# Performance work log

Hardware: AMD Instinct MI355X
Metric: run time of the kernel (lower is better)

The kernel has to match this reference:

```python
import jax, jax.numpy as jnp
import numpy as np

N_NODES = 50000
N_EDGES = 800000
N_GRAPHS = 256
D_IN = 128
D_HID = 128


def setup_inputs() -> dict:
    key = jax.random.key(0)
    ks = jax.random.split(key, 10)
    x = jax.random.normal(ks[0], (N_NODES, D_IN), dtype=jnp.float32)
    edge_index = jax.random.randint(ks[1], (2, N_EDGES), 0, N_NODES, dtype=jnp.int64)
    batch = jnp.sort(jax.random.randint(ks[2], (N_NODES,), 0, N_GRAPHS, dtype=jnp.int64))
    def lin(k, din, dout):
        s = 1.0 / np.sqrt(din)
        return jax.random.uniform(k, (din, dout), jnp.float32, -s, s)
    W1 = lin(ks[3], D_IN, D_HID); b1 = jnp.zeros((D_HID,), jnp.float32)
    W2 = lin(ks[4], D_HID, D_HID); b2 = jnp.zeros((D_HID,), jnp.float32)
    W3 = lin(ks[5], D_HID, D_HID); b3 = jnp.zeros((D_HID,), jnp.float32)
    return {"x": x, "edge_index": edge_index, "batch": batch,
            "W1": W1, "b1": b1, "W2": W2, "b2": b2, "W3": W3, "b3": b3}


def _gcn_norm(edge_index, num_nodes):
    # PyG gcn_norm with add_self_loops=True, edge_weight=1
    loops = jnp.arange(num_nodes, dtype=edge_index.dtype)
    src = jnp.concatenate([edge_index[0], loops])
    dst = jnp.concatenate([edge_index[1], loops])
    ones = jnp.ones(src.shape[0], jnp.float32)
    deg = jax.ops.segment_sum(ones, dst, num_segments=num_nodes)
    dinv = jnp.where(deg > 0, jax.lax.rsqrt(deg), 0.0)
    norm = dinv[src] * dinv[dst]
    return src, dst, norm


def _gcn_conv(x, src, dst, norm, W, b, num_nodes):
    h = x @ W                              # [N, dout] transform first
    msg = h[src] * norm[:, None]           # gather + scale  [E+N, dout]
    agg = jax.ops.segment_sum(msg, dst, num_segments=num_nodes)
    return agg + b


def reference(x, edge_index, batch, W1, b1, W2, b2, W3, b3):
    n = x.shape[0]
    src, dst, norm = _gcn_norm(edge_index, n)
    h = jax.nn.relu(_gcn_conv(x, src, dst, norm, W1, b1, n))
    h = jax.nn.relu(_gcn_conv(h, src, dst, norm, W2, b2, n))
    h = _gcn_conv(h, src, dst, norm, W3, b3, n)
    # global_mean_pool over batch ids
    sums = jax.ops.segment_sum(h, batch, num_segments=N_GRAPHS)
    cnts = jax.ops.segment_sum(jnp.ones((n,), jnp.float32), batch, num_segments=N_GRAPHS)
    return sums / jnp.maximum(cnts, 1.0)[:, None]
```

## Files before the change

kernel.cpp:

```cpp
#include <hip/hip_runtime.h>

#define N_NODES 50000
#define N_PAD   50048
#define N_EDGES 800000
#define N_GRAPHS 256
#define D 128
#define CAP 64
#define MFMA_GRID (N_PAD / 128)

#define NBUCK 196
#define BCAP  4608
#define EPB_I4 512
#define NBLK_A ((N_EDGES / 4 + EPB_I4 - 1) / EPB_I4)

typedef short bf16x8 __attribute__((ext_vector_type(8)));
typedef float f32x4  __attribute__((ext_vector_type(4)));

__device__ inline unsigned short f2bf(float f) {
    unsigned u = __float_as_uint(f);
    u += 0x7FFF + ((u >> 16) & 1);
    return (unsigned short)(u >> 16);
}
__device__ inline float bf2f(unsigned short b) { return __uint_as_float((unsigned)b << 16); }

__global__ __launch_bounds__(256) void k_pack(const float* __restrict__ W1, const float* __restrict__ W2,
                                              const float* __restrict__ W3, unsigned short* __restrict__ Wp) {
    int idx = blockIdx.x * 256 + threadIdx.x;
    if (idx >= 3 * D * D) return;
    int L = idx >> 14, rem = idx & 16383;
    int k = rem >> 7, n = rem & 127;
    const float* W = (L == 0) ? W1 : (L == 1) ? W2 : W3;
    float w = W[k * D + n];
    int kt = k >> 5, kg = (k >> 3) & 3, i = k & 7;
    int nt = n >> 4, ln = kg * 16 + (n & 15);
    size_t dst = (size_t)L * 32768 + ((size_t)(kt * 8 + nt) * 64 + ln) * 8 + i;
    unsigned short hi = f2bf(w);
    Wp[dst]         = hi;
    Wp[dst + 16384] = f2bf(w - bf2f(hi));
}


__global__ __launch_bounds__(256) void k_part(const int* __restrict__ ei, int* __restrict__ cursor,
                                              unsigned* __restrict__ buck) {
    __shared__ int hist[NBUCK];
    __shared__ int lbase[NBUCK];
    for (int i = threadIdx.x; i < NBUCK; i += 256) hist[i] = 0;
    __syncthreads();

    const int4* s4 = reinterpret_cast<const int4*>(ei);
    const int4* d4 = reinterpret_cast<const int4*>(ei + N_EDGES);
    int idx0 = blockIdx.x * EPB_I4 + threadIdx.x;
    int idx1 = idx0 + 256;
    bool v0 = idx0 < N_EDGES / 4, v1 = idx1 < N_EDGES / 4;
    int4 d0 = {}, d1 = {}, s0 = {}, s1 = {};
    if (v0) {
        d0 = d4[idx0]; s0 = s4[idx0];
        atomicAdd(&hist[d0.x >> 8], 1); atomicAdd(&hist[d0.y >> 8], 1);
        atomicAdd(&hist[d0.z >> 8], 1); atomicAdd(&hist[d0.w >> 8], 1);
    }
    if (v1) {
        d1 = d4[idx1]; s1 = s4[idx1];
        atomicAdd(&hist[d1.x >> 8], 1); atomicAdd(&hist[d1.y >> 8], 1);
        atomicAdd(&hist[d1.z >> 8], 1); atomicAdd(&hist[d1.w >> 8], 1);
    }
    __syncthreads();

    for (int i = threadIdx.x; i < NBUCK; i += 256)
        lbase[i] = atomicAdd(&cursor[i], hist[i]);
    __syncthreads();

    auto put = [&](int d, int s) {
        int b = d >> 8;
        int p = atomicAdd(&lbase[b], 1);
        if (p < BCAP) buck[(size_t)b * BCAP + p] = ((unsigned)(d & 255) << 16) | (unsigned)s;
    };
    if (v0) { put(d0.x, s0.x); put(d0.y, s0.y); put(d0.z, s0.z); put(d0.w, s0.w); }
    if (v1) { put(d1.x, s1.x); put(d1.y, s1.y); put(d1.z, s1.z); put(d1.w, s1.w); }
}


__global__ __launch_bounds__(256) void k_build(const unsigned* __restrict__ buck,
                                               const int* __restrict__ cursor,
                                               int* __restrict__ cnt, unsigned short* __restrict__ colu) {
    __shared__ int lcnt[256];
    int b = blockIdx.x;
    lcnt[threadIdx.x] = 0;
    __syncthreads();
    int nE = min(cursor[b], BCAP);
    const unsigned* bb = buck + (size_t)b * BCAP;
    for (int i = threadIdx.x; i < nE; i += 256) {
        unsigned v = bb[i];
        int dl = v >> 16, s = v & 0xFFFF;
        int p = atomicAdd(&lcnt[dl], 1);
        if (p < CAP) colu[(size_t)(b * 256 + dl) * CAP + p] = (unsigned short)s;
    }
    __syncthreads();
    int node = b * 256 + threadIdx.x;
    if (node < N_NODES) cnt[node] = lcnt[threadIdx.x];
}


template<bool F32IN>
__global__ __launch_bounds__(512) void k_mfma(const void* __restrict__ Ain,
                                              const unsigned short* __restrict__ Wp,
                                              const int* __restrict__ cnt,
                                              unsigned short* __restrict__ T) {
    __shared__ uint4 Wl[4096];
    const uint4* wp4 = reinterpret_cast<const uint4*>(Wp);
    for (int i = threadIdx.x; i < 4096; i += 512) Wl[i] = wp4[i];
    __syncthreads();

    int l  = threadIdx.x & 63;
    int wv = threadIdx.x >> 6;
    int row0 = blockIdx.x * 128 + wv * 16;
    int arow = row0 + (l & 15);
    int kchunk = l >> 4;

    f32x4 acc[8] = {};
    #pragma unroll
    for (int s = 0; s < 4; ++s) {
        bf16x8 af;
        if (F32IN) {
            float4 a0 = {}, a1 = {};
            if (arow < N_NODES) {
                const float* xr = (const float*)Ain + (size_t)arow * D + s * 32 + kchunk * 8;
                a0 = reinterpret_cast<const float4*>(xr)[0];
                a1 = reinterpret_cast<const float4*>(xr)[1];
            }
            unsigned short h[8] = { f2bf(a0.x), f2bf(a0.y), f2bf(a0.z), f2bf(a0.w),
                                    f2bf(a1.x), f2bf(a1.y), f2bf(a1.z), f2bf(a1.w) };
            __builtin_memcpy(&af, h, 16);
        } else {
            const unsigned short* ar = (const unsigned short*)Ain + (size_t)arow * D;
            uint4 av = reinterpret_cast<const uint4*>(ar)[s * 4 + kchunk];
            __builtin_memcpy(&af, &av, 16);
        }
        #pragma unroll
        for (int nt = 0; nt < 8; ++nt) {
            int f = s * 8 + nt;
            uint4 bh = Wl[f * 64 + l];
            uint4 bl = Wl[f * 64 + l + 2048];
            bf16x8 bhf, blf;
            __builtin_memcpy(&bhf, &bh, 16);
            __builtin_memcpy(&blf, &bl, 16);
            acc[nt] = __builtin_amdgcn_mfma_f32_16x16x32_bf16(af, bhf, acc[nt], 0, 0, 0);
            acc[nt] = __builtin_amdgcn_mfma_f32_16x16x32_bf16(af, blf, acc[nt], 0, 0, 0);
        }
    }

    int rbase = row0 + (l >> 4) * 4;
    int cr = l & 15;
    float sc[4];
    #pragma unroll
    for (int j = 0; j < 4; ++j) {
        int rr = rbase + j;
        sc[j] = (rr < N_NODES) ? rsqrtf((float)cnt[rr] + 1.f) : 0.f;
    }
    #pragma unroll
    for (int nt = 0; nt < 8; ++nt)
        #pragma unroll
        for (int j = 0; j < 4; ++j) {
            int rr = rbase + j;
            if (rr < N_NODES) T[(size_t)rr * D + nt * 16 + cr] = f2bf(acc[nt][j] * sc[j]);
        }
}


template<bool LAST>
__global__ __launch_bounds__(256) void k_agg(const unsigned* __restrict__ Tu,
                                             unsigned* __restrict__ Anext, const float* __restrict__ bias,
                                             const int* __restrict__ cnt, const unsigned short* __restrict__ colu) {
    int node = blockIdx.x * 4 + (threadIdx.x >> 6);
    int lane = threadIdx.x & 63;
    if (node >= N_NODES) return;

    int len = cnt[node];
    float dd = rsqrtf((float)len + 1.f);
    unsigned ts = Tu[(size_t)node * 64 + lane];
    float2 acc;
    acc.x = __uint_as_float(ts << 16);
    acc.y = __uint_as_float(ts & 0xFFFF0000u);

    const unsigned short* crow = colu + (size_t)node * CAP;
    int j = 0;
    for (; j + 8 <= len; j += 8) {
        uint4 c = *reinterpret_cast<const uint4*>(crow + j);
        int s0 = c.x & 0xFFFF, s1 = c.x >> 16;
        int s2 = c.y & 0xFFFF, s3 = c.y >> 16;
        int s4 = c.z & 0xFFFF, s5 = c.z >> 16;
        int s6 = c.w & 0xFFFF, s7 = c.w >> 16;
        unsigned t0 = Tu[(size_t)s0 * 64 + lane];
        unsigned t1 = Tu[(size_t)s1 * 64 + lane];
        unsigned t2 = Tu[(size_t)s2 * 64 + lane];
        unsigned t3 = Tu[(size_t)s3 * 64 + lane];
        unsigned t4 = Tu[(size_t)s4 * 64 + lane];
        unsigned t5 = Tu[(size_t)s5 * 64 + lane];
        unsigned t6 = Tu[(size_t)s6 * 64 + lane];
        unsigned t7 = Tu[(size_t)s7 * 64 + lane];
        acc.x += __uint_as_float(t0 << 16); acc.y += __uint_as_float(t0 & 0xFFFF0000u);
        acc.x += __uint_as_float(t1 << 16); acc.y += __uint_as_float(t1 & 0xFFFF0000u);
        acc.x += __uint_as_float(t2 << 16); acc.y += __uint_as_float(t2 & 0xFFFF0000u);
        acc.x += __uint_as_float(t3 << 16); acc.y += __uint_as_float(t3 & 0xFFFF0000u);
        acc.x += __uint_as_float(t4 << 16); acc.y += __uint_as_float(t4 & 0xFFFF0000u);
        acc.x += __uint_as_float(t5 << 16); acc.y += __uint_as_float(t5 & 0xFFFF0000u);
        acc.x += __uint_as_float(t6 << 16); acc.y += __uint_as_float(t6 & 0xFFFF0000u);
        acc.x += __uint_as_float(t7 << 16); acc.y += __uint_as_float(t7 & 0xFFFF0000u);
    }
    for (; j < len; ++j) {
        int s = crow[j];
        unsigned t0 = Tu[(size_t)s * 64 + lane];
        acc.x += __uint_as_float(t0 << 16); acc.y += __uint_as_float(t0 & 0xFFFF0000u);
    }

    acc.x *= dd; acc.y *= dd;
    if (!LAST) {
        acc.x = fmaxf(acc.x + bias[2 * lane], 0.f);
        acc.y = fmaxf(acc.y + bias[2 * lane + 1], 0.f);
    }
    Anext[(size_t)node * 64 + lane] = (unsigned)f2bf(acc.x) | ((unsigned)f2bf(acc.y) << 16);
}


__global__ __launch_bounds__(128) void k_pool(const unsigned short* __restrict__ AGGb,
                                              const float* __restrict__ b3,
                                              const int* __restrict__ batch, float* __restrict__ out) {
    int g = blockIdx.x;
    int c = threadIdx.x;
    int beg, end;
    { int lo = 0, hi = N_NODES; while (lo < hi) { int m = (lo + hi) >> 1; if (batch[m] < g) lo = m + 1; else hi = m; } beg = lo; }
    { int lo = beg, hi = N_NODES; while (lo < hi) { int m = (lo + hi) >> 1; if (batch[m] < g + 1) lo = m + 1; else hi = m; } end = lo; }
    float acc = 0.f;
    #pragma unroll 4
    for (int i = beg; i < end; ++i) acc += bf2f(AGGb[(size_t)i * D + c]);
    int n = end - beg;
    out[g * D + c] = (acc + (float)n * b3[c]) / (float)(n > 0 ? n : 1);
}


static inline size_t align256(size_t x) { return (x + 255) & ~(size_t)255; }

extern "C" void kernel_launch(void* const* d_in, const int* in_sizes, int n_in,
                              void* d_out, int out_size, void* d_ws, size_t ws_size,
                              hipStream_t stream) {
    const float* x    = (const float*)d_in[0];
    const int*  ei    = (const int*)d_in[1];
    const int*  batch = (const int*)d_in[2];
    const float* W1 = (const float*)d_in[3];
    const float* b1 = (const float*)d_in[4];
    const float* W2 = (const float*)d_in[5];
    const float* b2 = (const float*)d_in[6];
    const float* W3 = (const float*)d_in[7];
    const float* b3 = (const float*)d_in[8];
    float* out = (float*)d_out;

    char* ws = (char*)d_ws;
    size_t off = 0;
    auto alloc = [&](size_t bytes) { void* p = ws + off; off = align256(off + bytes); return p; };
    int*      cursor = (int*)     alloc((size_t)NBUCK * 4);
    unsigned* buck   = (unsigned*)alloc((size_t)NBUCK * BCAP * 4);
    int*      cnt    = (int*)     alloc((size_t)N_NODES * 4);
    unsigned short* colu = (unsigned short*)alloc((size_t)NBUCK * 256 * CAP * 2);
    unsigned short* Wp = (unsigned short*)alloc((size_t)3 * 32768 * 2);
    unsigned short* Ab = (unsigned short*)alloc((size_t)N_PAD * D * 2);
    unsigned short* T  = (unsigned short*)alloc((size_t)N_PAD * D * 2);
    (void)ws_size; (void)in_sizes; (void)n_in; (void)out_size;

    hipMemsetAsync(cursor, 0, (size_t)NBUCK * 4, stream);

    k_pack <<<(3 * D * D + 255) / 256, 256, 0, stream>>>(W1, W2, W3, Wp);
    k_part <<<NBLK_A, 256, 0, stream>>>(ei, cursor, buck);
    k_build<<<NBUCK, 256, 0, stream>>>(buck, cursor, cnt, colu);

    const int agg_grid = (N_NODES + 3) / 4;

    k_mfma<true ><<<MFMA_GRID, 512, 0, stream>>>(x,  Wp,         cnt, T);
    k_agg<false><<<agg_grid, 256, 0, stream>>>((const unsigned*)T, (unsigned*)Ab, b1, cnt, colu);
    k_mfma<false><<<MFMA_GRID, 512, 0, stream>>>(Ab, Wp + 32768, cnt, T);
    k_agg<false><<<agg_grid, 256, 0, stream>>>((const unsigned*)T, (unsigned*)Ab, b2, cnt, colu);
    k_mfma<false><<<MFMA_GRID, 512, 0, stream>>>(Ab, Wp + 65536, cnt, T);
    k_agg<true ><<<agg_grid, 256, 0, stream>>>((const unsigned*)T, (unsigned*)Ab, nullptr, cnt, colu);
    k_pool <<<N_GRAPHS, 128, 0, stream>>>(Ab, b3, batch, out);
}
```

Before: 276.3 us.

## Fuse last aggregation with mean pool, merge pack/partition, two nodes per wave

Merges the weight-pack and edge-partition kernels into one launch by splitting the block range. The aggregation kernel now handles two nodes per wavefront, interleaving their gathers so more loads are in flight. The final aggregation is fused into the pooling kernel: each graph block aggregates its own nodes and reduces directly, so the third layer's output is never written and reread. The cost is that the fused pool kernel runs only 256 blocks, one per graph, which may underuse the GPU for the last gather.

```diff
diff --git a/kernel.cpp b/kernel.cpp
--- a/kernel.cpp
+++ b/kernel.cpp
@@ -12,6 +12,7 @@
 #define BCAP  4608
 #define EPB_I4 512
 #define NBLK_A ((N_EDGES / 4 + EPB_I4 - 1) / EPB_I4)
+#define PACK_BLKS 192
 
 typedef short bf16x8 __attribute__((ext_vector_type(8)));
 typedef float f32x4  __attribute__((ext_vector_type(4)));
@@ -22,34 +23,59 @@
     return (unsigned short)(u >> 16);
 }
 __device__ inline float bf2f(unsigned short b) { return __uint_as_float((unsigned)b << 16); }
-
-__global__ __launch_bounds__(256) void k_pack(const float* __restrict__ W1, const float* __restrict__ W2,
-                                              const float* __restrict__ W3, unsigned short* __restrict__ Wp) {
-    int idx = blockIdx.x * 256 + threadIdx.x;
-    if (idx >= 3 * D * D) return;
-    int L = idx >> 14, rem = idx & 16383;
-    int k = rem >> 7, n = rem & 127;
-    const float* W = (L == 0) ? W1 : (L == 1) ? W2 : W3;
-    float w = W[k * D + n];
-    int kt = k >> 5, kg = (k >> 3) & 3, i = k & 7;
-    int nt = n >> 4, ln = kg * 16 + (n & 15);
-    size_t dst = (size_t)L * 32768 + ((size_t)(kt * 8 + nt) * 64 + ln) * 8 + i;
-    unsigned short hi = f2bf(w);
-    Wp[dst]         = hi;
-    Wp[dst + 16384] = f2bf(w - bf2f(hi));
-}
-
-
-__global__ __launch_bounds__(256) void k_part(const int* __restrict__ ei, int* __restrict__ cursor,
-                                              unsigned* __restrict__ buck) {
+__device__ inline float bflo(unsigned t) { return __uint_as_float(t << 16); }
+__device__ inline float bfhi(unsigned t) { return __uint_as_float(t & 0xFFFF0000u); }
+
+__device__ inline void gather8(const unsigned* __restrict__ Tu, const unsigned short* __restrict__ crow,
+                               int j, int lane, float2& acc) {
+    uint4 c = *reinterpret_cast<const uint4*>(crow + j);
+    unsigned t0 = Tu[(size_t)(c.x & 0xFFFF) * 64 + lane];
+    unsigned t1 = Tu[(size_t)(c.x >> 16)    * 64 + lane];
+    unsigned t2 = Tu[(size_t)(c.y & 0xFFFF) * 64 + lane];
+    unsigned t3 = Tu[(size_t)(c.y >> 16)    * 64 + lane];
+    unsigned t4 = Tu[(size_t)(c.z & 0xFFFF) * 64 + lane];
+    unsigned t5 = Tu[(size_t)(c.z >> 16)    * 64 + lane];
+    unsigned t6 = Tu[(size_t)(c.w & 0xFFFF) * 64 + lane];
+    unsigned t7 = Tu[(size_t)(c.w >> 16)    * 64 + lane];
+    acc.x += bflo(t0); acc.y += bfhi(t0);
+    acc.x += bflo(t1); acc.y += bfhi(t1);
+    acc.x += bflo(t2); acc.y += bfhi(t2);
+    acc.x += bflo(t3); acc.y += bfhi(t3);
+    acc.x += bflo(t4); acc.y += bfhi(t4);
+    acc.x += bflo(t5); acc.y += bfhi(t5);
+    acc.x += bflo(t6); acc.y += bfhi(t6);
+    acc.x += bflo(t7); acc.y += bfhi(t7);
+}
+
+
+__global__ __launch_bounds__(256) void k_packpart(const float* __restrict__ W1, const float* __restrict__ W2,
+                                                  const float* __restrict__ W3, unsigned short* __restrict__ Wp,
+                                                  const int* __restrict__ ei, int* __restrict__ cursor,
+                                                  unsigned* __restrict__ buck) {
+    if (blockIdx.x < PACK_BLKS) {
+        int idx = blockIdx.x * 256 + threadIdx.x;
+        int L = idx >> 14, rem = idx & 16383;
+        int k = rem >> 7, n = rem & 127;
+        const float* W = (L == 0) ? W1 : (L == 1) ? W2 : W3;
+        float w = W[k * D + n];
+        int kt = k >> 5, kg = (k >> 3) & 3, i = k & 7;
+        int nt = n >> 4, ln = kg * 16 + (n & 15);
+        size_t dst = (size_t)L * 32768 + ((size_t)(kt * 8 + nt) * 64 + ln) * 8 + i;
+        unsigned short hi = f2bf(w);
+        Wp[dst]         = hi;
+        Wp[dst + 16384] = f2bf(w - bf2f(hi));
+        return;
+    }
+
     __shared__ int hist[NBUCK];
     __shared__ int lbase[NBUCK];
     for (int i = threadIdx.x; i < NBUCK; i += 256) hist[i] = 0;
     __syncthreads();
 
+    int pb = blockIdx.x - PACK_BLKS;
     const int4* s4 = reinterpret_cast<const int4*>(ei);
     const int4* d4 = reinterpret_cast<const int4*>(ei + N_EDGES);
-    int idx0 = blockIdx.x * EPB_I4 + threadIdx.x;
+    int idx0 = pb * EPB_I4 + threadIdx.x;
     int idx1 = idx0 + 256;
     bool v0 = idx0 < N_EDGES / 4, v1 = idx1 < N_EDGES / 4;
     int4 d0 = {}, d1 = {}, s0 = {}, s1 = {};
@@ -166,74 +192,88 @@
 }
 
 
-template<bool LAST>
 __global__ __launch_bounds__(256) void k_agg(const unsigned* __restrict__ Tu,
                                              unsigned* __restrict__ Anext, const float* __restrict__ bias,
                                              const int* __restrict__ cnt, const unsigned short* __restrict__ colu) {
-    int node = blockIdx.x * 4 + (threadIdx.x >> 6);
+    int wid  = (blockIdx.x * 256 + threadIdx.x) >> 6;
     int lane = threadIdx.x & 63;
-    if (node >= N_NODES) return;
-
-    int len = cnt[node];
-    float dd = rsqrtf((float)len + 1.f);
-    unsigned ts = Tu[(size_t)node * 64 + lane];
-    float2 acc;
-    acc.x = __uint_as_float(ts << 16);
-    acc.y = __uint_as_float(ts & 0xFFFF0000u);
-
-    const unsigned short* crow = colu + (size_t)node * CAP;
+    int n0 = wid * 2;
+    if (n0 >= N_NODES) return;
+    int n1 = n0 + 1;
+
+    int len0 = cnt[n0], len1 = cnt[n1];
+    int lim0 = min(len0, CAP), lim1 = min(len1, CAP);
+    unsigned ts0 = Tu[(size_t)n0 * 64 + lane];
+    unsigned ts1 = Tu[(size_t)n1 * 64 + lane];
+    float2 A0, A1;
+    A0.x = bflo(ts0); A0.y = bfhi(ts0);
+    A1.x = bflo(ts1); A1.y = bfhi(ts1);
+
+    const unsigned short* r0 = colu + (size_t)n0 * CAP;
+    const unsigned short* r1 = colu + (size_t)n1 * CAP;
+    int m = min(lim0, lim1);
     int j = 0;
-    for (; j + 8 <= len; j += 8) {
-        uint4 c = *reinterpret_cast<const uint4*>(crow + j);
-        int s0 = c.x & 0xFFFF, s1 = c.x >> 16;
-        int s2 = c.y & 0xFFFF, s3 = c.y >> 16;
-        int s4 = c.z & 0xFFFF, s5 = c.z >> 16;
-        int s6 = c.w & 0xFFFF, s7 = c.w >> 16;
-        unsigned t0 = Tu[(size_t)s0 * 64 + lane];
-        unsigned t1 = Tu[(size_t)s1 * 64 + lane];
-        unsigned t2 = Tu[(size_t)s2 * 64 + lane];
-        unsigned t3 = Tu[(size_t)s3 * 64 + lane];
-        unsigned t4 = Tu[(size_t)s4 * 64 + lane];
-        unsigned t5 = Tu[(size_t)s5 * 64 + lane];
-        unsigned t6 = Tu[(size_t)s6 * 64 + lane];
-        unsigned t7 = Tu[(size_t)s7 * 64 + lane];
-        acc.x += __uint_as_float(t0 << 16); acc.y += __uint_as_float(t0 & 0xFFFF0000u);
-        acc.x += __uint_as_float(t1 << 16); acc.y += __uint_as_float(t1 & 0xFFFF0000u);
-        acc.x += __uint_as_float(t2 << 16); acc.y += __uint_as_float(t2 & 0xFFFF0000u);
-        acc.x += __uint_as_float(t3 << 16); acc.y += __uint_as_float(t3 & 0xFFFF0000u);
-        acc.x += __uint_as_float(t4 << 16); acc.y += __uint_as_float(t4 & 0xFFFF0000u);
-        acc.x += __uint_as_float(t5 << 16); acc.y += __uint_as_float(t5 & 0xFFFF0000u);
-        acc.x += __uint_as_float(t6 << 16); acc.y += __uint_as_float(t6 & 0xFFFF0000u);
-        acc.x += __uint_as_float(t7 << 16); acc.y += __uint_as_float(t7 & 0xFFFF0000u);
-    }
-    for (; j < len; ++j) {
-        int s = crow[j];
-        unsigned t0 = Tu[(size_t)s * 64 + lane];
-        acc.x += __uint_as_float(t0 << 16); acc.y += __uint_as_float(t0 & 0xFFFF0000u);
-    }
-
-    acc.x *= dd; acc.y *= dd;
-    if (!LAST) {
-        acc.x = fmaxf(acc.x + bias[2 * lane], 0.f);
-        acc.y = fmaxf(acc.y + bias[2 * lane + 1], 0.f);
-    }
-    Anext[(size_t)node * 64 + lane] = (unsigned)f2bf(acc.x) | ((unsigned)f2bf(acc.y) << 16);
-}
-
-
-__global__ __launch_bounds__(128) void k_pool(const unsigned short* __restrict__ AGGb,
-                                              const float* __restrict__ b3,
-                                              const int* __restrict__ batch, float* __restrict__ out) {
+    for (; j + 8 <= m; j += 8) {
+        gather8(Tu, r0, j, lane, A0);
+        gather8(Tu, r1, j, lane, A1);
+    }
+    int ja = j;
+    for (; ja + 8 <= lim0; ja += 8) gather8(Tu, r0, ja, lane, A0);
+    for (; ja < lim0; ++ja) { unsigned t = Tu[(size_t)r0[ja] * 64 + lane]; A0.x += bflo(t); A0.y += bfhi(t); }
+    int jb = j;
+    for (; jb + 8 <= lim1; jb += 8) gather8(Tu, r1, jb, lane, A1);
+    for (; jb < lim1; ++jb) { unsigned t = Tu[(size_t)r1[jb] * 64 + lane]; A1.x += bflo(t); A1.y += bfhi(t); }
+
+    float dd0 = rsqrtf((float)len0 + 1.f);
+    float dd1 = rsqrtf((float)len1 + 1.f);
+    float bx = bias[2 * lane], by = bias[2 * lane + 1];
+    float r0x = fmaxf(A0.x * dd0 + bx, 0.f), r0y = fmaxf(A0.y * dd0 + by, 0.f);
+    float r1x = fmaxf(A1.x * dd1 + bx, 0.f), r1y = fmaxf(A1.y * dd1 + by, 0.f);
+    Anext[(size_t)n0 * 64 + lane] = (unsigned)f2bf(r0x) | ((unsigned)f2bf(r0y) << 16);
+    Anext[(size_t)n1 * 64 + lane] = (unsigned)f2bf(r1x) | ((unsigned)f2bf(r1y) << 16);
+}
+
+
+__global__ __launch_bounds__(1024) void k_aggpool(const unsigned* __restrict__ Tu,
+                                                  const int* __restrict__ cnt,
+                                                  const unsigned short* __restrict__ colu,
+                                                  const int* __restrict__ batch,
+                                                  const float* __restrict__ b3,
+                                                  float* __restrict__ out) {
     int g = blockIdx.x;
-    int c = threadIdx.x;
     int beg, end;
     { int lo = 0, hi = N_NODES; while (lo < hi) { int m = (lo + hi) >> 1; if (batch[m] < g) lo = m + 1; else hi = m; } beg = lo; }
     { int lo = beg, hi = N_NODES; while (lo < hi) { int m = (lo + hi) >> 1; if (batch[m] < g + 1) lo = m + 1; else hi = m; } end = lo; }
-    float acc = 0.f;
-    #pragma unroll 4
-    for (int i = beg; i < end; ++i) acc += bf2f(AGGb[(size_t)i * D + c]);
-    int n = end - beg;
-    out[g * D + c] = (acc + (float)n * b3[c]) / (float)(n > 0 ? n : 1);
+    int lane = threadIdx.x & 63, wv = threadIdx.x >> 6;
+
+    float2 psum = make_float2(0.f, 0.f);
+    for (int node = beg + wv; node < end; node += 16) {
+        int len = cnt[node];
+        int lim = min(len, CAP);
+        unsigned ts = Tu[(size_t)node * 64 + lane];
+        float2 acc;
+        acc.x = bflo(ts); acc.y = bfhi(ts);
+        const unsigned short* crow = colu + (size_t)node * CAP;
+        int j = 0;
+        for (; j + 8 <= lim; j += 8) gather8(Tu, crow, j, lane, acc);
+        for (; j < lim; ++j) { unsigned t = Tu[(size_t)crow[j] * 64 + lane]; acc.x += bflo(t); acc.y += bfhi(t); }
+        float dd = rsqrtf((float)len + 1.f);
+        psum.x += acc.x * dd;
+        psum.y += acc.y * dd;
+    }
+
+    __shared__ float2 red[16][64];
+    red[wv][lane] = psum;
+    __syncthreads();
+    if (wv == 0) {
+        float2 s = red[0][lane];
+        #pragma unroll
+        for (int w = 1; w < 16; ++w) { s.x += red[w][lane].x; s.y += red[w][lane].y; }
+        int n = end - beg;
+        float inv = 1.f / (float)(n > 0 ? n : 1);
+        out[g * D + 2 * lane]     = (s.x + (float)n * b3[2 * lane])     * inv;
+        out[g * D + 2 * lane + 1] = (s.y + (float)n * b3[2 * lane + 1]) * inv;
+    }
 }
 
 
@@ -267,17 +307,15 @@
 
     hipMemsetAsync(cursor, 0, (size_t)NBUCK * 4, stream);
 
-    k_pack <<<(3 * D * D + 255) / 256, 256, 0, stream>>>(W1, W2, W3, Wp);
-    k_part <<<NBLK_A, 256, 0, stream>>>(ei, cursor, buck);
-    k_build<<<NBUCK, 256, 0, stream>>>(buck, cursor, cnt, colu);
-
-    const int agg_grid = (N_NODES + 3) / 4;
+    k_packpart<<<PACK_BLKS + NBLK_A, 256, 0, stream>>>(W1, W2, W3, Wp, ei, cursor, buck);
+    k_build   <<<NBUCK, 256, 0, stream>>>(buck, cursor, cnt, colu);
+
+    const int agg_grid = (N_NODES / 2 + 3) / 4;
 
     k_mfma<true ><<<MFMA_GRID, 512, 0, stream>>>(x,  Wp,         cnt, T);
-    k_agg<false><<<agg_grid, 256, 0, stream>>>((const unsigned*)T, (unsigned*)Ab, b1, cnt, colu);
+    k_agg        <<<agg_grid, 256, 0, stream>>>((const unsigned*)T, (unsigned*)Ab, b1, cnt, colu);
     k_mfma<false><<<MFMA_GRID, 512, 0, stream>>>(Ab, Wp + 32768, cnt, T);
-    k_agg<false><<<agg_grid, 256, 0, stream>>>((const unsigned*)T, (unsigned*)Ab, b2, cnt, colu);
+    k_agg        <<<agg_grid, 256, 0, stream>>>((const unsigned*)T, (unsigned*)Ab, b2, cnt, colu);
     k_mfma<false><<<MFMA_GRID, 512, 0, stream>>>(Ab, Wp + 65536, cnt, T);
-    k_agg<true ><<<agg_grid, 256, 0, stream>>>((const unsigned*)T, (unsigned*)Ab, nullptr, cnt, colu);
-    k_pool <<<N_GRAPHS, 128, 0, stream>>>(Ab, b3, batch, out);
-}
+    k_aggpool    <<<N_GRAPHS, 1024, 0, stream>>>((const unsigned*)T, cnt, colu, batch, b3, out);
+}
```

After: 280.8 us. About the same (+1.6%).
